# Kernel tuning notes

Measured on AMD Instinct MI355X. Metric: run time of the kernel, lower is better.

## Reference

```python
import jax, jax.numpy as jnp
import numpy as np

ODE_UNFOLDS = 6
EPS = 1e-8
B, S, N = 512, 256, 256


def setup_inputs() -> dict:
    key = jax.random.key(0)
    ks = jax.random.split(key, 16)
    u = lambda k, shape, lo, hi: jax.random.uniform(k, shape, jnp.float32, lo, hi)
    erev_signs = lambda k, shape: jnp.where(jax.random.bernoulli(k, 0.5, shape), 1.0, -1.0).astype(jnp.float32)
    return {
        "input": jax.random.normal(ks[0], (B, S), jnp.float32),
        "hx": jax.random.normal(ks[1], (B, N), jnp.float32),
        "ts": jax.random.uniform(ks[2], (B,), jnp.float32),
        "gleak": u(ks[3], (N,), 0.001, 1.0),
        "vleak": u(ks[4], (N,), -0.2, 0.2),
        "cm": u(ks[5], (N,), 0.4, 0.6),
        "sigma": u(ks[6], (N, N), 3.0, 8.0),
        "mu": u(ks[7], (N, N), 0.3, 0.8),
        "w": u(ks[8], (N, N), 0.001, 1.0),
        "erev": erev_signs(ks[9], (N, N)),
        "sensory_sigma": u(ks[10], (S, N), 3.0, 8.0),
        "sensory_mu": u(ks[11], (S, N), 0.3, 0.8),
        "sensory_w": u(ks[12], (S, N), 0.001, 1.0),
        "sensory_erev": erev_signs(ks[13], (S, N)),
        "input_w": jnp.ones((S,), jnp.float32),
        "input_b": jnp.zeros((S,), jnp.float32),
    }


def reference(input, hx, ts, gleak, vleak, cm, sigma, mu, w, erev,
              sensory_sigma, sensory_mu, sensory_w, sensory_erev,
              input_w, input_b):
    # map inputs (softplus in the original is Identity)
    inputs = input * input_w + input_b                      # (B, S)
    # sensory synapse: broadcast sigmoid over (B, S, N)
    sens_act = sensory_w * jax.nn.sigmoid(
        sensory_sigma * (inputs[:, :, None] - sensory_mu))  # (B, S, N)
    w_num_s = jnp.sum(sens_act * sensory_erev, axis=1)      # (B, N)
    w_den_s = jnp.sum(sens_act, axis=1)                     # (B, N)

    ts_col = ts.reshape(-1, 1)                              # (B, 1)
    cm_t = cm[None, :] / ((ts_col + 1.0) / ODE_UNFOLDS)     # (B, N)

    def step(v_pre, _):
        # (B, N, N) neuron-to-neuron synapse activation
        w_act = w * jax.nn.sigmoid(sigma * (v_pre[:, :, None] - mu))
        w_num = jnp.sum(w_act * erev, axis=1) + w_num_s     # (B, N)
        w_den = jnp.sum(w_act, axis=1) + w_den_s            # (B, N)
        numerator = cm_t * v_pre + gleak * vleak + w_num
        denominator = cm_t + gleak + w_den
        return numerator / (denominator + EPS), None

    v_pre, _ = jax.lax.scan(step, hx, None, length=ODE_UNFOLDS)
    return v_pre
```

## Files before the change

### kernel.cpp

```cpp
#include <hip/hip_runtime.h>


#define LOG2E 1.4426950408889634f
#define EXP2_RAW(x) __builtin_amdgcn_exp2f(x)
#define RCP_RAW(x) __builtin_amdgcn_rcpf(x)

typedef float f2 __attribute__((ext_vector_type(2)));
typedef _Float16 h2 __attribute__((ext_vector_type(2)));

constexpr int Bb = 512;
constexpr int Ss = 256;
constexpr int Nn = 256;
constexpr int UNFOLDS = 6;
constexpr float EPS = 1e-8f;
constexpr int PLANE = 16384;

struct alignas(16) HQ { h2 a[4]; };
struct alignas(8)  WQ { _Float16 w[4]; };

__global__ __launch_bounds__(256) void pack_kernel(
    const float* __restrict__ sg, const float* __restrict__ mu,
    const float* __restrict__ w, const float* __restrict__ er,
    const float* __restrict__ ssg, const float* __restrict__ smu,
    const float* __restrict__ sw, const float* __restrict__ ser,
    HQ* __restrict__ pH, WQ* __restrict__ pW,
    HQ* __restrict__ sH, WQ* __restrict__ sW) {
  int idx = blockIdx.x * 256 + threadIdx.x;
  int b = (idx >> 8) * 1024 + (idx & 255);
  HQ hq; WQ wq;
#pragma unroll
  for (int k = 0; k < 4; ++k) {
    int o = b + k * 256;
    float a = sg[o] * LOG2E;
    hq.a[k] = h2{(_Float16)a, (_Float16)(a * mu[o])};
    wq.w[k] = (_Float16)(w[o] * er[o]);
  }
  pH[idx] = hq; pW[idx] = wq;
#pragma unroll
  for (int k = 0; k < 4; ++k) {
    int o = b + k * 256;
    float a = ssg[o] * LOG2E;
    hq.a[k] = h2{(_Float16)a, (_Float16)(a * smu[o])};
    wq.w[k] = (_Float16)(sw[o] * ser[o]);
  }
  sH[idx] = hq; sW[idx] = wq;
}

struct Acc8 {
  f2 na0, nb0, da0, db0, na1, nb1, da1, db1;
};

template <bool PACKED>
__device__ __forceinline__ Acc8 pass_accum(
    const HQ* __restrict__ pH, const WQ* __restrict__ pW,
    const float* __restrict__ rS, const float* __restrict__ rM,
    const float* __restrict__ rW, const float* __restrict__ rE,
    const float* x0p, const float* x1p, int c, int j) {
  Acc8 acc;
  acc.na0 = 0.f; acc.nb0 = 0.f; acc.da0 = 0.f; acc.db0 = 0.f;
  acc.na1 = 0.f; acc.nb1 = 0.f; acc.da1 = 0.f; acc.db1 = 0.f;
  const int pb0 = c * 4096 + j;
  HQ H; WQ W;
  if constexpr (PACKED) { H = pH[pb0]; W = pW[pb0]; }
#pragma unroll 2
  for (int ip = 0; ip < 16; ++ip) {
    HQ Hn; WQ Wn;
    f2 a01, a23, m01, m23, wn01, wn23;
    if constexpr (PACKED) {
      const int ni = pb0 + (((ip + 1) & 15) << 8);
      Hn = pH[ni]; Wn = pW[ni];
      a01 = f2{(float)H.a[0].x, (float)H.a[1].x};
      a23 = f2{(float)H.a[2].x, (float)H.a[3].x};
      m01 = f2{(float)H.a[0].y, (float)H.a[1].y};
      m23 = f2{(float)H.a[2].y, (float)H.a[3].y};
      wn01 = f2{(float)W.w[0], (float)W.w[1]};
      wn23 = f2{(float)W.w[2], (float)W.w[3]};
    } else {
      const int b = (c * 64 + ip * 4) * Nn + j;
      a01 = f2{rS[b] * LOG2E, rS[b + 256] * LOG2E};
      a23 = f2{rS[b + 512] * LOG2E, rS[b + 768] * LOG2E};
      m01 = f2{a01.x * rM[b], a01.y * rM[b + 256]};
      m23 = f2{a23.x * rM[b + 512], a23.y * rM[b + 768]};
      wn01 = f2{rW[b] * rE[b], rW[b + 256] * rE[b + 256]};
      wn23 = f2{rW[b + 512] * rE[b + 512], rW[b + 768] * rE[b + 768]};
    }
    const f2 wd01 = {__builtin_fabsf(wn01.x), __builtin_fabsf(wn01.y)};
    const f2 wd23 = {__builtin_fabsf(wn23.x), __builtin_fabsf(wn23.y)};
    const int ib = c * 64 + ip * 4;
    const float4 xq0 = *reinterpret_cast<const float4*>(&x0p[ib]);
    const float4 xq1 = *reinterpret_cast<const float4*>(&x1p[ib]);

    {
      const f2 x01 = {xq0.x, xq0.y}, x23 = {xq0.z, xq0.w};
      const f2 y01 = m01 - a01 * x01;
      const f2 y23 = m23 - a23 * x23;
      f2 s01, s23;
      s01.x = RCP_RAW(1.f + EXP2_RAW(y01.x));
      s01.y = RCP_RAW(1.f + EXP2_RAW(y01.y));
      s23.x = RCP_RAW(1.f + EXP2_RAW(y23.x));
      s23.y = RCP_RAW(1.f + EXP2_RAW(y23.y));
      acc.na0 += wn01 * s01; acc.nb0 += wn23 * s23;
      acc.da0 += wd01 * s01; acc.db0 += wd23 * s23;
    }
    {
      const f2 x01 = {xq1.x, xq1.y}, x23 = {xq1.z, xq1.w};
      const f2 y01 = m01 - a01 * x01;
      const f2 y23 = m23 - a23 * x23;
      f2 s01, s23;
      s01.x = RCP_RAW(1.f + EXP2_RAW(y01.x));
      s01.y = RCP_RAW(1.f + EXP2_RAW(y01.y));
      s23.x = RCP_RAW(1.f + EXP2_RAW(y23.x));
      s23.y = RCP_RAW(1.f + EXP2_RAW(y23.y));
      acc.na1 += wn01 * s01; acc.nb1 += wn23 * s23;
      acc.da1 += wd01 * s01; acc.db1 += wd23 * s23;
    }
    if constexpr (PACKED) { H = Hn; W = Wn; }
  }
  return acc;
}

template <bool PACKED>
__global__ __launch_bounds__(1024, 1) void ltc_kernel(
    const float* __restrict__ input, const float* __restrict__ hx,
    const float* __restrict__ ts, const float* __restrict__ gleak,
    const float* __restrict__ vleak, const float* __restrict__ cm,
    const float* __restrict__ input_w, const float* __restrict__ input_b,
    const HQ* __restrict__ pH, const WQ* __restrict__ pW,
    const HQ* __restrict__ sH, const WQ* __restrict__ sW,
    const float* __restrict__ sigmaP, const float* __restrict__ muP,
    const float* __restrict__ wP, const float* __restrict__ erevP,
    const float* __restrict__ ssigmaP, const float* __restrict__ smuP,
    const float* __restrict__ swP, const float* __restrict__ serevP,
    float* __restrict__ out) {
  __shared__ alignas(16) float v_lds[2][Nn];
  __shared__ alignas(16) float inp_lds[2][Ss];
  __shared__ alignas(16) float4 red[1024];

  const int tid = threadIdx.x;
  const int j = tid & 255;
  const int c = tid >> 8;
  const int b0 = blockIdx.x * 2;

  if (tid < 512) {
    int r = tid >> 8, s = tid & 255;
    inp_lds[r][s] = input[(b0 + r) * Ss + s] * input_w[s] + input_b[s];
    v_lds[r][s] = hx[(b0 + r) * Nn + s];
  }
  __syncthreads();

  {
    Acc8 acc = pass_accum<PACKED>(sH, sW, ssigmaP, smuP, swP, serevP,
                                  &inp_lds[0][0], &inp_lds[1][0], c, j);
    red[tid] = make_float4(acc.na0.x + acc.na0.y + acc.nb0.x + acc.nb0.y,
                           acc.da0.x + acc.da0.y + acc.db0.x + acc.db0.y,
                           acc.na1.x + acc.na1.y + acc.nb1.x + acc.nb1.y,
                           acc.da1.x + acc.da1.y + acc.db1.x + acc.db1.y);
  }
  __syncthreads();

  float snum0 = 0.f, sden0 = 0.f, snum1 = 0.f, sden1 = 0.f;
  float cmt0 = 0.f, cmt1 = 0.f, glj = 0.f, glvl = 0.f;
  if (c == 0) {
    float4 a = red[j], b = red[256 + j], cc = red[512 + j], d = red[768 + j];
    snum0 = a.x + b.x + cc.x + d.x;
    sden0 = a.y + b.y + cc.y + d.y;
    snum1 = a.z + b.z + cc.z + d.z;
    sden1 = a.w + b.w + cc.w + d.w;
    glj = gleak[j];
    glvl = glj * vleak[j];
    float cmj = cm[j];
    cmt0 = cmj / ((ts[b0] + 1.f) / (float)UNFOLDS);
    cmt1 = cmj / ((ts[b0 + 1] + 1.f) / (float)UNFOLDS);
  }
  __syncthreads();

  float vo0 = 0.f, vo1 = 0.f;
  for (int step = 0; step < UNFOLDS; ++step) {
    Acc8 acc = pass_accum<PACKED>(pH, pW, sigmaP, muP, wP, erevP,
                                  &v_lds[0][0], &v_lds[1][0], c, j);
    red[tid] = make_float4(acc.na0.x + acc.na0.y + acc.nb0.x + acc.nb0.y,
                           acc.da0.x + acc.da0.y + acc.db0.x + acc.db0.y,
                           acc.na1.x + acc.na1.y + acc.nb1.x + acc.nb1.y,
                           acc.da1.x + acc.da1.y + acc.db1.x + acc.db1.y);
    __syncthreads();
    if (c == 0) {
      float4 a = red[j], b = red[256 + j], cc = red[512 + j], d = red[768 + j];
      float num0 = a.x + b.x + cc.x + d.x + snum0;
      float den0 = a.y + b.y + cc.y + d.y + sden0;
      float num1 = a.z + b.z + cc.z + d.z + snum1;
      float den1 = a.w + b.w + cc.w + d.w + sden1;
      float v0 = v_lds[0][j], v1 = v_lds[1][j];
      vo0 = (cmt0 * v0 + glvl + num0) / (cmt0 + glj + den0 + EPS);
      vo1 = (cmt1 * v1 + glvl + num1) / (cmt1 + glj + den1 + EPS);
      v_lds[0][j] = vo0;
      v_lds[1][j] = vo1;
    }
    __syncthreads();
  }

  if (c == 0) {
    out[b0 * Nn + j] = vo0;
    out[(b0 + 1) * Nn + j] = vo1;
  }
}

extern "C" void kernel_launch(void* const* d_in, const int* in_sizes, int n_in,
                              void* d_out, int out_size, void* d_ws, size_t ws_size,
                              hipStream_t stream) {
  const float* input   = (const float*)d_in[0];
  const float* hx      = (const float*)d_in[1];
  const float* ts      = (const float*)d_in[2];
  const float* gleak   = (const float*)d_in[3];
  const float* vleak   = (const float*)d_in[4];
  const float* cm      = (const float*)d_in[5];
  const float* sigma   = (const float*)d_in[6];
  const float* mu      = (const float*)d_in[7];
  const float* w       = (const float*)d_in[8];
  const float* erev    = (const float*)d_in[9];
  const float* ssigma  = (const float*)d_in[10];
  const float* smu     = (const float*)d_in[11];
  const float* sw      = (const float*)d_in[12];
  const float* serev   = (const float*)d_in[13];
  const float* input_w = (const float*)d_in[14];
  const float* input_b = (const float*)d_in[15];
  float* out = (float*)d_out;

  const size_t need = (size_t)PLANE * (sizeof(HQ) * 2 + sizeof(WQ) * 2);
  if (ws_size >= need) {
    HQ* pH = (HQ*)d_ws;
    HQ* sH = pH + PLANE;
    WQ* pW = (WQ*)(sH + PLANE);
    WQ* sW = pW + PLANE;
    pack_kernel<<<PLANE / 256, 256, 0, stream>>>(sigma, mu, w, erev, ssigma,
                                                 smu, sw, serev, pH, pW, sH, sW);
    ltc_kernel<true><<<Bb / 2, 1024, 0, stream>>>(
        input, hx, ts, gleak, vleak, cm, input_w, input_b, pH, pW, sH, sW,
        sigma, mu, w, erev, ssigma, smu, sw, serev, out);
  } else {
    ltc_kernel<false><<<Bb / 2, 1024, 0, stream>>>(
        input, hx, ts, gleak, vleak, cm, input_w, input_b,
        nullptr, nullptr, nullptr, nullptr,
        sigma, mu, w, erev, ssigma, smu, sw, serev, out);
  }
}
```

Before: 151.7 us.

## Use one batch row per block with quad-lane shuffle reduction

Each block now handles one batch element instead of two, and the grid doubles to match. The four partial sums over the presynaptic index are assigned to adjacent lanes and combined with xor shuffles. This replaces the LDS reduction buffer and one barrier per ODE step, and the voltage vector is double-buffered in LDS. Per-block weight reuse is halved, global weight loads become strided across lane quads, and the raised launch-bounds occupancy hint may force register pressure.

Result: slower. 280.8 us (+85.1%).

```diff
diff --git a/kernel.cpp b/kernel.cpp
--- a/kernel.cpp
+++ b/kernel.cpp
@@ -46,28 +46,22 @@
   sH[idx] = hq; sW[idx] = wq;
 }
 
-struct Acc8 {
-  f2 na0, nb0, da0, db0, na1, nb1, da1, db1;
-};
-
 template <bool PACKED>
-__device__ __forceinline__ Acc8 pass_accum(
+__device__ __forceinline__ f2 pass_accum(
     const HQ* __restrict__ pH, const WQ* __restrict__ pW,
     const float* __restrict__ rS, const float* __restrict__ rM,
     const float* __restrict__ rW, const float* __restrict__ rE,
-    const float* x0p, const float* x1p, int c, int j) {
-  Acc8 acc;
-  acc.na0 = 0.f; acc.nb0 = 0.f; acc.da0 = 0.f; acc.db0 = 0.f;
-  acc.na1 = 0.f; acc.nb1 = 0.f; acc.da1 = 0.f; acc.db1 = 0.f;
-  const int pb0 = c * 4096 + j;
+    const float* __restrict__ xp, int c, int j) {
+  f2 na01 = 0.f, na23 = 0.f, da01 = 0.f, da23 = 0.f;
+  const int q0 = (c << 4) * 256 + j;
   HQ H; WQ W;
-  if constexpr (PACKED) { H = pH[pb0]; W = pW[pb0]; }
+  if constexpr (PACKED) { H = pH[q0]; W = pW[q0]; }
 #pragma unroll 2
   for (int ip = 0; ip < 16; ++ip) {
     HQ Hn; WQ Wn;
     f2 a01, a23, m01, m23, wn01, wn23;
     if constexpr (PACKED) {
-      const int ni = pb0 + (((ip + 1) & 15) << 8);
+      const int ni = q0 + ((((ip + 1) & 15)) << 8);
       Hn = pH[ni]; Wn = pW[ni];
       a01 = f2{(float)H.a[0].x, (float)H.a[1].x};
       a23 = f2{(float)H.a[2].x, (float)H.a[3].x};
@@ -86,41 +80,25 @@
     }
     const f2 wd01 = {__builtin_fabsf(wn01.x), __builtin_fabsf(wn01.y)};
     const f2 wd23 = {__builtin_fabsf(wn23.x), __builtin_fabsf(wn23.y)};
-    const int ib = c * 64 + ip * 4;
-    const float4 xq0 = *reinterpret_cast<const float4*>(&x0p[ib]);
-    const float4 xq1 = *reinterpret_cast<const float4*>(&x1p[ib]);
-
-    {
-      const f2 x01 = {xq0.x, xq0.y}, x23 = {xq0.z, xq0.w};
-      const f2 y01 = m01 - a01 * x01;
-      const f2 y23 = m23 - a23 * x23;
-      f2 s01, s23;
-      s01.x = RCP_RAW(1.f + EXP2_RAW(y01.x));
-      s01.y = RCP_RAW(1.f + EXP2_RAW(y01.y));
-      s23.x = RCP_RAW(1.f + EXP2_RAW(y23.x));
-      s23.y = RCP_RAW(1.f + EXP2_RAW(y23.y));
-      acc.na0 += wn01 * s01; acc.nb0 += wn23 * s23;
-      acc.da0 += wd01 * s01; acc.db0 += wd23 * s23;
-    }
-    {
-      const f2 x01 = {xq1.x, xq1.y}, x23 = {xq1.z, xq1.w};
-      const f2 y01 = m01 - a01 * x01;
-      const f2 y23 = m23 - a23 * x23;
-      f2 s01, s23;
-      s01.x = RCP_RAW(1.f + EXP2_RAW(y01.x));
-      s01.y = RCP_RAW(1.f + EXP2_RAW(y01.y));
-      s23.x = RCP_RAW(1.f + EXP2_RAW(y23.x));
-      s23.y = RCP_RAW(1.f + EXP2_RAW(y23.y));
-      acc.na1 += wn01 * s01; acc.nb1 += wn23 * s23;
-      acc.da1 += wd01 * s01; acc.db1 += wd23 * s23;
-    }
+    const float4 xq = *reinterpret_cast<const float4*>(&xp[c * 64 + ip * 4]);
+    const f2 x01 = {xq.x, xq.y}, x23 = {xq.z, xq.w};
+    const f2 y01 = m01 - a01 * x01;
+    const f2 y23 = m23 - a23 * x23;
+    f2 s01, s23;
+    s01.x = RCP_RAW(1.f + EXP2_RAW(y01.x));
+    s01.y = RCP_RAW(1.f + EXP2_RAW(y01.y));
+    s23.x = RCP_RAW(1.f + EXP2_RAW(y23.x));
+    s23.y = RCP_RAW(1.f + EXP2_RAW(y23.y));
+    na01 += wn01 * s01; na23 += wn23 * s23;
+    da01 += wd01 * s01; da23 += wd23 * s23;
     if constexpr (PACKED) { H = Hn; W = Wn; }
   }
-  return acc;
+  return f2{na01.x + na01.y + na23.x + na23.y,
+            da01.x + da01.y + da23.x + da23.y};
 }
 
 template <bool PACKED>
-__global__ __launch_bounds__(1024, 1) void ltc_kernel(
+__global__ __launch_bounds__(1024, 8) void ltc_kernel(
     const float* __restrict__ input, const float* __restrict__ hx,
     const float* __restrict__ ts, const float* __restrict__ gleak,
     const float* __restrict__ vleak, const float* __restrict__ cm,
@@ -133,75 +111,51 @@
     const float* __restrict__ swP, const float* __restrict__ serevP,
     float* __restrict__ out) {
   __shared__ alignas(16) float v_lds[2][Nn];
-  __shared__ alignas(16) float inp_lds[2][Ss];
-  __shared__ alignas(16) float4 red[1024];
+  __shared__ alignas(16) float inp_lds[Ss];
 
   const int tid = threadIdx.x;
-  const int j = tid & 255;
-  const int c = tid >> 8;
-  const int b0 = blockIdx.x * 2;
+  const int j = tid >> 2;
+  const int c = tid & 3;
+  const int b0 = blockIdx.x;
 
-  if (tid < 512) {
-    int r = tid >> 8, s = tid & 255;
-    inp_lds[r][s] = input[(b0 + r) * Ss + s] * input_w[s] + input_b[s];
-    v_lds[r][s] = hx[(b0 + r) * Nn + s];
+  if (tid < 256) {
+    inp_lds[tid] = input[b0 * Ss + tid] * input_w[tid] + input_b[tid];
+    v_lds[0][tid] = hx[b0 * Nn + tid];
   }
+
+  float vreg = hx[b0 * Nn + j];
+  const float glj = gleak[j];
+  const float glvl = glj * vleak[j];
+  const float cmt = cm[j] / ((ts[b0] + 1.f) / (float)UNFOLDS);
+
   __syncthreads();
 
+  float snum, sden;
   {
-    Acc8 acc = pass_accum<PACKED>(sH, sW, ssigmaP, smuP, swP, serevP,
-                                  &inp_lds[0][0], &inp_lds[1][0], c, j);
-    red[tid] = make_float4(acc.na0.x + acc.na0.y + acc.nb0.x + acc.nb0.y,
-                           acc.da0.x + acc.da0.y + acc.db0.x + acc.db0.y,
-                           acc.na1.x + acc.na1.y + acc.nb1.x + acc.nb1.y,
-                           acc.da1.x + acc.da1.y + acc.db1.x + acc.db1.y);
+    f2 s = pass_accum<PACKED>(sH, sW, ssigmaP, smuP, swP, serevP,
+                              &inp_lds[0], c, j);
+    snum = s.x; sden = s.y;
+    snum += __shfl_xor(snum, 1); snum += __shfl_xor(snum, 2);
+    sden += __shfl_xor(sden, 1); sden += __shfl_xor(sden, 2);
   }
-  __syncthreads();
 
-  float snum0 = 0.f, sden0 = 0.f, snum1 = 0.f, sden1 = 0.f;
-  float cmt0 = 0.f, cmt1 = 0.f, glj = 0.f, glvl = 0.f;
-  if (c == 0) {
-    float4 a = red[j], b = red[256 + j], cc = red[512 + j], d = red[768 + j];
-    snum0 = a.x + b.x + cc.x + d.x;
-    sden0 = a.y + b.y + cc.y + d.y;
-    snum1 = a.z + b.z + cc.z + d.z;
-    sden1 = a.w + b.w + cc.w + d.w;
-    glj = gleak[j];
-    glvl = glj * vleak[j];
-    float cmj = cm[j];
-    cmt0 = cmj / ((ts[b0] + 1.f) / (float)UNFOLDS);
-    cmt1 = cmj / ((ts[b0 + 1] + 1.f) / (float)UNFOLDS);
-  }
-  __syncthreads();
-
-  float vo0 = 0.f, vo1 = 0.f;
+  int cur = 0;
+  float vo = vreg;
   for (int step = 0; step < UNFOLDS; ++step) {
-    Acc8 acc = pass_accum<PACKED>(pH, pW, sigmaP, muP, wP, erevP,
-                                  &v_lds[0][0], &v_lds[1][0], c, j);
-    red[tid] = make_float4(acc.na0.x + acc.na0.y + acc.nb0.x + acc.nb0.y,
-                           acc.da0.x + acc.da0.y + acc.db0.x + acc.db0.y,
-                           acc.na1.x + acc.na1.y + acc.nb1.x + acc.nb1.y,
-                           acc.da1.x + acc.da1.y + acc.db1.x + acc.db1.y);
-    __syncthreads();
-    if (c == 0) {
-      float4 a = red[j], b = red[256 + j], cc = red[512 + j], d = red[768 + j];
-      float num0 = a.x + b.x + cc.x + d.x + snum0;
-      float den0 = a.y + b.y + cc.y + d.y + sden0;
-      float num1 = a.z + b.z + cc.z + d.z + snum1;
-      float den1 = a.w + b.w + cc.w + d.w + sden1;
-      float v0 = v_lds[0][j], v1 = v_lds[1][j];
-      vo0 = (cmt0 * v0 + glvl + num0) / (cmt0 + glj + den0 + EPS);
-      vo1 = (cmt1 * v1 + glvl + num1) / (cmt1 + glj + den1 + EPS);
-      v_lds[0][j] = vo0;
-      v_lds[1][j] = vo1;
-    }
+    f2 a = pass_accum<PACKED>(pH, pW, sigmaP, muP, wP, erevP,
+                              &v_lds[cur][0], c, j);
+    float num = a.x, den = a.y;
+    num += __shfl_xor(num, 1); num += __shfl_xor(num, 2);
+    den += __shfl_xor(den, 1); den += __shfl_xor(den, 2);
+    num += snum; den += sden;
+    vo = (cmt * vreg + glvl + num) / (cmt + glj + den + EPS);
+    if (c == 0) v_lds[cur ^ 1][j] = vo;
+    vreg = vo;
+    cur ^= 1;
     __syncthreads();
   }
 
-  if (c == 0) {
-    out[b0 * Nn + j] = vo0;
-    out[(b0 + 1) * Nn + j] = vo1;
-  }
+  if (c == 0) out[b0 * Nn + j] = vo;
 }
 
 extern "C" void kernel_launch(void* const* d_in, const int* in_sizes, int n_in,
@@ -233,11 +187,11 @@
     WQ* sW = pW + PLANE;
     pack_kernel<<<PLANE / 256, 256, 0, stream>>>(sigma, mu, w, erev, ssigma,
                                                  smu, sw, serev, pH, pW, sH, sW);
-    ltc_kernel<true><<<Bb / 2, 1024, 0, stream>>>(
+    ltc_kernel<true><<<Bb, 1024, 0, stream>>>(
         input, hx, ts, gleak, vleak, cm, input_w, input_b, pH, pW, sH, sW,
         sigma, mu, w, erev, ssigma, smu, sw, serev, out);
   } else {
-    ltc_kernel<false><<<Bb / 2, 1024, 0, stream>>>(
+    ltc_kernel<false><<<Bb, 1024, 0, stream>>>(
         input, hx, ts, gleak, vleak, cm, input_w, input_b,
         nullptr, nullptr, nullptr, nullptr,
         sigma, mu, w, erev, ssigma, smu, sw, serev, out);
```
